# Kernel optimization log

Hardware: AMD Instinct MI355X
Metric: run time of the kernel (lower is better)

Reference implementation:

```python
import jax, jax.numpy as jnp
import numpy as np

N = 131072      # total nodes
B = 512         # number of graphs
F_DIM = 512     # in_channels
H = F_DIM // 2  # score_net hidden
RATIO = 0.5
MARGIN = 0.5
TOPK_LOSS_WEIGHT = 0.2


def setup_inputs() -> dict:
    key = jax.random.key(0)
    k1, k2, k3 = jax.random.split(key, 3)
    x = jax.random.normal(k1, (N, F_DIM), dtype=jnp.float32)
    # sorted segment ids: equal-sized graphs of N // B nodes
    batch = (jnp.arange(N) // (N // B)).astype(jnp.int32)
    W1 = jax.random.normal(k2, (F_DIM, H), dtype=jnp.float32) / np.sqrt(F_DIM).astype(np.float32)
    b1 = jnp.zeros((H,), dtype=jnp.float32)
    W2 = jax.random.normal(k3, (H, 1), dtype=jnp.float32) / np.sqrt(H).astype(np.float32)
    b2 = jnp.zeros((1,), dtype=jnp.float32)
    return {"x": x, "batch": batch, "W1": W1, "b1": b1, "W2": W2, "b2": b2}


def reference(x, batch, W1, b1, W2, b2):
    # scores = score_net(x).squeeze(-1)   [N]
    scores = (jax.nn.relu(x @ W1 + b1) @ W2 + b2)[:, 0]

    # per-graph node counts and k = max(1, int(ratio * n_i))
    counts = jax.ops.segment_sum(jnp.ones((N,), dtype=scores.dtype), batch, num_segments=B)
    k = jnp.maximum(1, jnp.floor(RATIO * counts).astype(jnp.int32))  # [B]

    # segmented top-k via lexsort: sort by (batch asc, score desc)
    order = jnp.lexsort((-scores, batch))          # [N] permutation
    b_sorted = batch[order]
    starts = jnp.cumsum(counts) - counts           # exclusive-cumsum segment starts
    rank = jnp.arange(N, dtype=counts.dtype) - starts[b_sorted]  # rank within graph (0 = highest score)
    sel_sorted = rank < k[b_sorted].astype(counts.dtype)
    selected_mask = jnp.zeros((N,), dtype=bool).at[order].set(sel_sorted)

    # global_add_pool over selected nodes
    m = selected_mask.astype(x.dtype)
    x_pooled = jax.ops.segment_sum(x * m[:, None], batch, num_segments=B)  # [B, F]

    # margin regularization loss per graph
    sel_cnt = jax.ops.segment_sum(m, batch, num_segments=B)
    sel_sum = jax.ops.segment_sum(scores * m, batch, num_segments=B)
    tot_sum = jax.ops.segment_sum(scores, batch, num_segments=B)
    uns_cnt = counts - sel_cnt
    sel_mean = sel_sum / jnp.maximum(sel_cnt, 1.0)
    uns_mean = (tot_sum - sel_sum) / jnp.maximum(uns_cnt, 1.0)
    per_graph = jnp.where(uns_cnt > 0, jax.nn.relu(MARGIN - (sel_mean - uns_mean)), 0.0)
    topk_loss = per_graph.sum() / B * TOPK_LOSS_WEIGHT

    return x_pooled, topk_loss, selected_mask
```

## Files before the change

### kernel.cpp

```cpp
#include <hip/hip_runtime.h>

#define N_NODES 131072
#define BGRAPHS 512
#define FDIM    512
#define HDIM    256
#define NPG     256
#define KSEL    128
#define STAGES  16
#define STAGE_UNITS 3072
#define STAGE_BYTES (STAGE_UNITS * 16)

typedef __attribute__((ext_vector_type(8)))  short bf16x8;
typedef __attribute__((ext_vector_type(16))) float f32x16;

__device__ __forceinline__ unsigned short bf16_rne(float f, float* back) {
    unsigned u = __float_as_uint(f);
    unsigned r = u + 0x7FFFu + ((u >> 16) & 1u);
    unsigned short h = (unsigned short)(r >> 16);
    *back = __uint_as_float(((unsigned)h) << 16);
    return h;
}

__global__ __launch_bounds__(256)
void split_w1_kernel(const float* __restrict__ W1, unsigned short* __restrict__ wsB)
{
    const int uid  = blockIdx.x * 256 + threadIdx.x;
    const int lane = uid & 63;
    int t = uid >> 6;
    const int nt = t & 7;  t >>= 3;
    const int q  = t & 1;  t >>= 1;
    const int p  = t % 3;
    const int s  = t / 3;
    const int n  = nt * 32 + (lane & 31);
    const int k0 = s * 32 + q * 16 + (lane >> 5) * 8;

    bf16x8 v;
    #pragma unroll
    for (int j = 0; j < 8; ++j) {
        float w = W1[(size_t)(k0 + j) * HDIM + n];
        float f1, f2, f3;
        unsigned short h1 = bf16_rne(w, &f1);
        float r1 = w - f1;
        unsigned short h2 = bf16_rne(r1, &f2);
        float r2 = r1 - f2;
        unsigned short h3 = bf16_rne(r2, &f3);
        v[j] = (short)(p == 0 ? h1 : (p == 1 ? h2 : h3));
    }
    *(bf16x8*)(wsB + (size_t)uid * 8) = v;
}

__global__ __launch_bounds__(512, 2)
void fused_kernel(const float* __restrict__ x,
                  const unsigned short* __restrict__ wsB,
                  const float* __restrict__ b1, const float* __restrict__ W2,
                  const float* __restrict__ b2,
                  float* __restrict__ pooled, float* __restrict__ mask_out,
                  float* __restrict__ loss_per_g)
{
    __shared__ unsigned short ldsB[STAGE_BYTES / 2];
    __shared__ float Sp[2][NPG];
    __shared__ float sv[NPG];
    __shared__ int   selr[KSEL];
    __shared__ float redT[NPG];
    __shared__ float redS[NPG];

    const int g    = blockIdx.x;
    const int tid  = threadIdx.x;
    const int lane = tid & 63;
    const int wv   = tid >> 6;
    const int wy   = wv & 3;
    const int wx   = wv >> 2;
    const int l31  = lane & 31;
    const int lh   = lane >> 5;
    const int m_base = g * NPG + wy * 64;

    f32x16 acc[2][4];
    #pragma unroll
    for (int a = 0; a < 2; ++a)
        #pragma unroll
        for (int b = 0; b < 4; ++b)
            #pragma unroll
            for (int r = 0; r < 16; ++r) acc[a][b][r] = 0.f;

    for (int s = 0; s < STAGES; ++s) {
        __syncthreads();
        const unsigned short* src = wsB + (size_t)s * (STAGE_BYTES / 2);
        #pragma unroll
        for (int i = 0; i < 6; ++i) {
            const int unit = i * 512 + tid;
            __builtin_amdgcn_global_load_lds(
                (const __attribute__((address_space(1))) unsigned int*)(src + (size_t)unit * 8),
                (__attribute__((address_space(3))) unsigned int*)(ldsB + unit * 8),
                16, 0, 0);
        }
        __syncthreads();

        #pragma unroll
        for (int q = 0; q < 2; ++q) {
            float4 xa[2], xb[2];
            #pragma unroll
            for (int mt = 0; mt < 2; ++mt) {
                const int row = m_base + mt * 32 + l31;
                const float* xp = x + (size_t)row * FDIM + s * 32 + q * 16 + lh * 8;
                xa[mt] = *(const float4*)xp;
                xb[mt] = *(const float4*)(xp + 4);
            }
            const bf16x8* bfp = (const bf16x8*)ldsB;
            bf16x8 Bh[4], Bm[4], Bl[4];
            #pragma unroll
            for (int nt = 0; nt < 4; ++nt) {
                const int nn = wx * 4 + nt;
                Bh[nt] = bfp[((0 * 2 + q) * 8 + nn) * 64 + lane];
                Bm[nt] = bfp[((1 * 2 + q) * 8 + nn) * 64 + lane];
                Bl[nt] = bfp[((2 * 2 + q) * 8 + nn) * 64 + lane];
            }
            #pragma unroll
            for (int mt = 0; mt < 2; ++mt) {
                float v[8] = {xa[mt].x, xa[mt].y, xa[mt].z, xa[mt].w,
                              xb[mt].x, xb[mt].y, xb[mt].z, xb[mt].w};
                bf16x8 Ah, Am, Al;
                #pragma unroll
                for (int j = 0; j < 8; ++j) {
                    float f1, f2, f3;
                    unsigned short h1 = bf16_rne(v[j], &f1);
                    float r1 = v[j] - f1;
                    unsigned short h2 = bf16_rne(r1, &f2);
                    float r2 = r1 - f2;
                    unsigned short h3 = bf16_rne(r2, &f3);
                    Ah[j] = (short)h1; Am[j] = (short)h2; Al[j] = (short)h3;
                }
                #pragma unroll
                for (int nt = 0; nt < 4; ++nt) {
                    acc[mt][nt] = __builtin_amdgcn_mfma_f32_32x32x16_bf16(Ah, Bh[nt], acc[mt][nt], 0, 0, 0);
                    acc[mt][nt] = __builtin_amdgcn_mfma_f32_32x32x16_bf16(Ah, Bm[nt], acc[mt][nt], 0, 0, 0);
                    acc[mt][nt] = __builtin_amdgcn_mfma_f32_32x32x16_bf16(Am, Bh[nt], acc[mt][nt], 0, 0, 0);
                    acc[mt][nt] = __builtin_amdgcn_mfma_f32_32x32x16_bf16(Ah, Bl[nt], acc[mt][nt], 0, 0, 0);
                    acc[mt][nt] = __builtin_amdgcn_mfma_f32_32x32x16_bf16(Al, Bh[nt], acc[mt][nt], 0, 0, 0);
                    acc[mt][nt] = __builtin_amdgcn_mfma_f32_32x32x16_bf16(Am, Bm[nt], acc[mt][nt], 0, 0, 0);
                }
            }
        }
    }

    float bb[4], ww[4];
    #pragma unroll
    for (int nt = 0; nt < 4; ++nt) {
        const int c = wx * 128 + nt * 32 + l31;
        bb[nt] = b1[c];
        ww[nt] = W2[c];
    }
    #pragma unroll
    for (int mt = 0; mt < 2; ++mt) {
        float pr[16];
        #pragma unroll
        for (int r = 0; r < 16; ++r) pr[r] = 0.f;
        #pragma unroll
        for (int nt = 0; nt < 4; ++nt)
            #pragma unroll
            for (int r = 0; r < 16; ++r) {
                float h = acc[mt][nt][r] + bb[nt];
                h = h > 0.f ? h : 0.f;
                pr[r] = fmaf(h, ww[nt], pr[r]);
            }
        #pragma unroll
        for (int mask = 1; mask <= 16; mask <<= 1)
            #pragma unroll
            for (int r = 0; r < 16; ++r)
                pr[r] += __shfl_xor(pr[r], mask);
        if (l31 == 0) {
            #pragma unroll
            for (int r = 0; r < 16; ++r) {
                const int row = wy * 64 + mt * 32 + (r & 3) + 8 * (r >> 2) + 4 * lh;
                Sp[wx][row] = pr[r];
            }
        }
    }
    __syncthreads();

    float sc = 0.f;
    if (tid < NPG) {
        sc = b2[0] + Sp[0][tid] + Sp[1][tid];
        sv[tid] = sc;
    }
    __syncthreads();

    bool sel = false;
    if (tid < NPG) {
        int rank = 0;
        for (int j = 0; j < NPG; ++j) {
            const float sj = sv[j];
            rank += (sj > sc || (sj == sc && j < tid)) ? 1 : 0;
        }
        sel = rank < KSEL;
        mask_out[g * NPG + tid] = sel ? 1.0f : 0.0f;
        if (sel) selr[rank] = tid;
        redT[tid] = sc;
        redS[tid] = sel ? sc : 0.f;
    }
    __syncthreads();

    for (int off = 128; off > 0; off >>= 1) {
        if (tid < off) { redT[tid] += redT[tid + off]; redS[tid] += redS[tid + off]; }
        __syncthreads();
    }
    if (tid == 0) {
        const float tot = redT[0], ssum = redS[0];
        const float sel_mean = ssum * (1.0f / KSEL);
        const float uns_mean = (tot - ssum) * (1.0f / (NPG - KSEL));
        const float v = 0.5f - (sel_mean - uns_mean);
        loss_per_g[g] = v > 0.f ? v : 0.f;
    }

    const int col = tid;
    const float* __restrict__ xg = x + (size_t)g * NPG * FDIM;
    float a0 = 0.f, a1 = 0.f, a2 = 0.f, a3 = 0.f;
    #pragma unroll 4
    for (int n = 0; n < KSEL; n += 4) {
        a0 += xg[(size_t)selr[n + 0] * FDIM + col];
        a1 += xg[(size_t)selr[n + 1] * FDIM + col];
        a2 += xg[(size_t)selr[n + 2] * FDIM + col];
        a3 += xg[(size_t)selr[n + 3] * FDIM + col];
    }
    pooled[g * FDIM + col] = (a0 + a1) + (a2 + a3);
}

__global__ __launch_bounds__(256)
void loss_kernel(const float* __restrict__ loss_per_g, float* __restrict__ out_loss)
{
    __shared__ float red[256];
    const int t = threadIdx.x;
    red[t] = loss_per_g[t] + loss_per_g[t + 256];
    __syncthreads();
    for (int off = 128; off > 0; off >>= 1) {
        if (t < off) red[t] += red[t + off];
        __syncthreads();
    }
    if (t == 0) out_loss[0] = red[0] * (0.2f / BGRAPHS);
}

extern "C" void kernel_launch(void* const* d_in, const int* in_sizes, int n_in,
                              void* d_out, int out_size, void* d_ws, size_t ws_size,
                              hipStream_t stream)
{
    const float* x  = (const float*)d_in[0];
    const float* W1 = (const float*)d_in[2];
    const float* b1 = (const float*)d_in[3];
    const float* W2 = (const float*)d_in[4];
    const float* b2 = (const float*)d_in[5];

    float* out    = (float*)d_out;
    float* pooled = out;
    float* loss   = out + BGRAPHS * FDIM;
    float* mask   = loss + 1;

    float* loss_g       = (float*)d_ws;
    unsigned short* wsB = (unsigned short*)((char*)d_ws + 4096);

    split_w1_kernel<<<192, 256, 0, stream>>>(W1, wsB);
    fused_kernel<<<BGRAPHS, 512, 0, stream>>>(x, wsB, b1, W2, b2,
                                              pooled, mask, loss_g);
    loss_kernel<<<1, 256, 0, stream>>>(loss_g, loss);
}
```

Before: 506.4 us.

## Double-buffer W1 stages and split x into bf16 planes once in LDS

The W1 bf16 stage buffer is now double-buffered, so loads for the next K-stage are issued before the current stage's MFMAs. Each x element is now split into three bf16 planes once per block and stored in padded LDS tiles. Previously the two column-half waves each split the same x elements, so this removes duplicated conversion work and duplicated global loads. The cost is much more LDS per block (about 157 KB), which likely allows only one block per CU instead of two. The W1 prepack layout is also reordered so each stage's planes sit next to each other.

```diff
diff --git a/kernel.cpp b/kernel.cpp
--- a/kernel.cpp
+++ b/kernel.cpp
@@ -7,8 +7,9 @@
 #define NPG     256
 #define KSEL    128
 #define STAGES  16
-#define STAGE_UNITS 3072
-#define STAGE_BYTES (STAGE_UNITS * 16)
+#define BSTAGE_SHORTS 24576
+#define A_ROW   40
+#define A_PLANE (NPG * A_ROW)
 
 typedef __attribute__((ext_vector_type(8)))  short bf16x8;
 typedef __attribute__((ext_vector_type(16))) float f32x16;
@@ -28,9 +29,9 @@
     const int lane = uid & 63;
     int t = uid >> 6;
     const int nt = t & 7;  t >>= 3;
-    const int q  = t & 1;  t >>= 1;
-    const int p  = t % 3;
-    const int s  = t / 3;
+    const int p  = t % 3;  t /= 3;
+    const int q  = t & 1;
+    const int s  = t >> 1;
     const int n  = nt * 32 + (lane & 31);
     const int k0 = s * 32 + q * 16 + (lane >> 5) * 8;
 
@@ -57,12 +58,8 @@
                   float* __restrict__ pooled, float* __restrict__ mask_out,
                   float* __restrict__ loss_per_g)
 {
-    __shared__ unsigned short ldsB[STAGE_BYTES / 2];
-    __shared__ float Sp[2][NPG];
-    __shared__ float sv[NPG];
-    __shared__ int   selr[KSEL];
-    __shared__ float redT[NPG];
-    __shared__ float redS[NPG];
+    __shared__ __attribute__((aligned(16))) unsigned char smem[2 * 49152 + 3 * A_PLANE * 2];
+    unsigned short* ldsA = (unsigned short*)(smem + 2 * 49152);
 
     const int g    = blockIdx.x;
     const int tid  = threadIdx.x;
@@ -72,7 +69,10 @@
     const int wx   = wv >> 2;
     const int l31  = lane & 31;
     const int lh   = lane >> 5;
-    const int m_base = g * NPG + wy * 64;
+
+    const int r  = tid >> 1;
+    const int hf = tid & 1;
+    const float* aptr = x + ((size_t)(g * NPG + r)) * FDIM + hf * 16;
 
     f32x16 acc[2][4];
     #pragma unroll
@@ -80,55 +80,96 @@
         #pragma unroll
         for (int b = 0; b < 4; ++b)
             #pragma unroll
-            for (int r = 0; r < 16; ++r) acc[a][b][r] = 0.f;
-
-    for (int s = 0; s < STAGES; ++s) {
-        __syncthreads();
-        const unsigned short* src = wsB + (size_t)s * (STAGE_BYTES / 2);
+            for (int rr = 0; rr < 16; ++rr) acc[a][b][rr] = 0.f;
+
+    float4 pf0, pf1, pf2, pf3;
+
+    pf0 = *(const float4*)(aptr + 0);
+    pf1 = *(const float4*)(aptr + 4);
+    pf2 = *(const float4*)(aptr + 8);
+    pf3 = *(const float4*)(aptr + 12);
+    {
+        const unsigned short* src = wsB;
         #pragma unroll
         for (int i = 0; i < 6; ++i) {
             const int unit = i * 512 + tid;
             __builtin_amdgcn_global_load_lds(
                 (const __attribute__((address_space(1))) unsigned int*)(src + (size_t)unit * 8),
-                (__attribute__((address_space(3))) unsigned int*)(ldsB + unit * 8),
+                (__attribute__((address_space(3))) unsigned int*)((unsigned short*)smem + unit * 8),
                 16, 0, 0);
         }
-        __syncthreads();
-
+    }
+    {
+        float v[16] = {pf0.x, pf0.y, pf0.z, pf0.w, pf1.x, pf1.y, pf1.z, pf1.w,
+                       pf2.x, pf2.y, pf2.z, pf2.w, pf3.x, pf3.y, pf3.z, pf3.w};
+        unsigned short H[16], M[16], L[16];
+        #pragma unroll
+        for (int j = 0; j < 16; ++j) {
+            float f1, f2, f3;
+            H[j] = bf16_rne(v[j], &f1);
+            float r1 = v[j] - f1;
+            M[j] = bf16_rne(r1, &f2);
+            float r2 = r1 - f2;
+            L[j] = bf16_rne(r2, &f3);
+        }
+        const int base = r * A_ROW + hf * 16;
+        const unsigned short* P[3] = {H, M, L};
+        #pragma unroll
+        for (int p = 0; p < 3; ++p) {
+            const unsigned short* s8 = P[p];
+            uint4 u0, u1;
+            u0.x = (unsigned)s8[0] | ((unsigned)s8[1] << 16);
+            u0.y = (unsigned)s8[2] | ((unsigned)s8[3] << 16);
+            u0.z = (unsigned)s8[4] | ((unsigned)s8[5] << 16);
+            u0.w = (unsigned)s8[6] | ((unsigned)s8[7] << 16);
+            u1.x = (unsigned)s8[8] | ((unsigned)s8[9] << 16);
+            u1.y = (unsigned)s8[10] | ((unsigned)s8[11] << 16);
+            u1.z = (unsigned)s8[12] | ((unsigned)s8[13] << 16);
+            u1.w = (unsigned)s8[14] | ((unsigned)s8[15] << 16);
+            uint4* dst = (uint4*)(ldsA + p * A_PLANE + base);
+            dst[0] = u0;
+            dst[1] = u1;
+        }
+    }
+    __syncthreads();
+
+    for (int s = 0; s < STAGES; ++s) {
+        if (s < STAGES - 1) {
+            const unsigned short* src = wsB + (size_t)(s + 1) * BSTAGE_SHORTS;
+            unsigned short* dstB = (unsigned short*)smem + ((s + 1) & 1) * BSTAGE_SHORTS;
+            #pragma unroll
+            for (int i = 0; i < 6; ++i) {
+                const int unit = i * 512 + tid;
+                __builtin_amdgcn_global_load_lds(
+                    (const __attribute__((address_space(1))) unsigned int*)(src + (size_t)unit * 8),
+                    (__attribute__((address_space(3))) unsigned int*)(dstB + unit * 8),
+                    16, 0, 0);
+            }
+            const float* ap = aptr + (s + 1) * 32;
+            pf0 = *(const float4*)(ap + 0);
+            pf1 = *(const float4*)(ap + 4);
+            pf2 = *(const float4*)(ap + 8);
+            pf3 = *(const float4*)(ap + 12);
+        }
+
+        const bf16x8* bfp = (const bf16x8*)((unsigned short*)smem + (s & 1) * BSTAGE_SHORTS);
         #pragma unroll
         for (int q = 0; q < 2; ++q) {
-            float4 xa[2], xb[2];
-            #pragma unroll
-            for (int mt = 0; mt < 2; ++mt) {
-                const int row = m_base + mt * 32 + l31;
-                const float* xp = x + (size_t)row * FDIM + s * 32 + q * 16 + lh * 8;
-                xa[mt] = *(const float4*)xp;
-                xb[mt] = *(const float4*)(xp + 4);
-            }
-            const bf16x8* bfp = (const bf16x8*)ldsB;
             bf16x8 Bh[4], Bm[4], Bl[4];
             #pragma unroll
             for (int nt = 0; nt < 4; ++nt) {
                 const int nn = wx * 4 + nt;
-                Bh[nt] = bfp[((0 * 2 + q) * 8 + nn) * 64 + lane];
-                Bm[nt] = bfp[((1 * 2 + q) * 8 + nn) * 64 + lane];
-                Bl[nt] = bfp[((2 * 2 + q) * 8 + nn) * 64 + lane];
+                Bh[nt] = bfp[((q * 3 + 0) * 8 + nn) * 64 + lane];
+                Bm[nt] = bfp[((q * 3 + 1) * 8 + nn) * 64 + lane];
+                Bl[nt] = bfp[((q * 3 + 2) * 8 + nn) * 64 + lane];
             }
             #pragma unroll
             for (int mt = 0; mt < 2; ++mt) {
-                float v[8] = {xa[mt].x, xa[mt].y, xa[mt].z, xa[mt].w,
-                              xb[mt].x, xb[mt].y, xb[mt].z, xb[mt].w};
-                bf16x8 Ah, Am, Al;
-                #pragma unroll
-                for (int j = 0; j < 8; ++j) {
-                    float f1, f2, f3;
-                    unsigned short h1 = bf16_rne(v[j], &f1);
-                    float r1 = v[j] - f1;
-                    unsigned short h2 = bf16_rne(r1, &f2);
-                    float r2 = r1 - f2;
-                    unsigned short h3 = bf16_rne(r2, &f3);
-                    Ah[j] = (short)h1; Am[j] = (short)h2; Al[j] = (short)h3;
-                }
+                const int m = wy * 64 + mt * 32 + l31;
+                const int aoff = m * A_ROW + q * 16 + lh * 8;
+                bf16x8 Ah = *(const bf16x8*)(ldsA + 0 * A_PLANE + aoff);
+                bf16x8 Am = *(const bf16x8*)(ldsA + 1 * A_PLANE + aoff);
+                bf16x8 Al = *(const bf16x8*)(ldsA + 2 * A_PLANE + aoff);
                 #pragma unroll
                 for (int nt = 0; nt < 4; ++nt) {
                     acc[mt][nt] = __builtin_amdgcn_mfma_f32_32x32x16_bf16(Ah, Bh[nt], acc[mt][nt], 0, 0, 0);
@@ -140,7 +181,48 @@
                 }
             }
         }
-    }
+        __syncthreads();
+
+        if (s < STAGES - 1) {
+            float v[16] = {pf0.x, pf0.y, pf0.z, pf0.w, pf1.x, pf1.y, pf1.z, pf1.w,
+                           pf2.x, pf2.y, pf2.z, pf2.w, pf3.x, pf3.y, pf3.z, pf3.w};
+            unsigned short H[16], M[16], L[16];
+            #pragma unroll
+            for (int j = 0; j < 16; ++j) {
+                float f1, f2, f3;
+                H[j] = bf16_rne(v[j], &f1);
+                float r1 = v[j] - f1;
+                M[j] = bf16_rne(r1, &f2);
+                float r2 = r1 - f2;
+                L[j] = bf16_rne(r2, &f3);
+            }
+            const int base = r * A_ROW + hf * 16;
+            const unsigned short* P[3] = {H, M, L};
+            #pragma unroll
+            for (int p = 0; p < 3; ++p) {
+                const unsigned short* s8 = P[p];
+                uint4 u0, u1;
+                u0.x = (unsigned)s8[0] | ((unsigned)s8[1] << 16);
+                u0.y = (unsigned)s8[2] | ((unsigned)s8[3] << 16);
+                u0.z = (unsigned)s8[4] | ((unsigned)s8[5] << 16);
+                u0.w = (unsigned)s8[6] | ((unsigned)s8[7] << 16);
+                u1.x = (unsigned)s8[8] | ((unsigned)s8[9] << 16);
+                u1.y = (unsigned)s8[10] | ((unsigned)s8[11] << 16);
+                u1.z = (unsigned)s8[12] | ((unsigned)s8[13] << 16);
+                u1.w = (unsigned)s8[14] | ((unsigned)s8[15] << 16);
+                uint4* dst = (uint4*)(ldsA + p * A_PLANE + base);
+                dst[0] = u0;
+                dst[1] = u1;
+            }
+        }
+        __syncthreads();
+    }
+
+    float* Sp   = (float*)smem;
+    float* sv   = Sp + 2 * NPG;
+    int*   selr = (int*)(sv + NPG);
+    float* redT = (float*)(selr + KSEL);
+    float* redS = redT + NPG;
 
     float bb[4], ww[4];
     #pragma unroll
@@ -153,25 +235,25 @@
     for (int mt = 0; mt < 2; ++mt) {
         float pr[16];
         #pragma unroll
-        for (int r = 0; r < 16; ++r) pr[r] = 0.f;
+        for (int rr = 0; rr < 16; ++rr) pr[rr] = 0.f;
         #pragma unroll
         for (int nt = 0; nt < 4; ++nt)
             #pragma unroll
-            for (int r = 0; r < 16; ++r) {
-                float h = acc[mt][nt][r] + bb[nt];
+            for (int rr = 0; rr < 16; ++rr) {
+                float h = acc[mt][nt][rr] + bb[nt];
                 h = h > 0.f ? h : 0.f;
-                pr[r] = fmaf(h, ww[nt], pr[r]);
+                pr[rr] = fmaf(h, ww[nt], pr[rr]);
             }
         #pragma unroll
         for (int mask = 1; mask <= 16; mask <<= 1)
             #pragma unroll
-            for (int r = 0; r < 16; ++r)
-                pr[r] += __shfl_xor(pr[r], mask);
+            for (int rr = 0; rr < 16; ++rr)
+                pr[rr] += __shfl_xor(pr[rr], mask);
         if (l31 == 0) {
             #pragma unroll
-            for (int r = 0; r < 16; ++r) {
-                const int row = wy * 64 + mt * 32 + (r & 3) + 8 * (r >> 2) + 4 * lh;
-                Sp[wx][row] = pr[r];
+            for (int rr = 0; rr < 16; ++rr) {
+                const int row = wy * 64 + mt * 32 + (rr & 3) + 8 * (rr >> 2) + 4 * lh;
+                Sp[wx * NPG + row] = pr[rr];
             }
         }
     }
@@ -179,19 +261,18 @@
 
     float sc = 0.f;
     if (tid < NPG) {
-        sc = b2[0] + Sp[0][tid] + Sp[1][tid];
+        sc = b2[0] + Sp[tid] + Sp[NPG + tid];
         sv[tid] = sc;
     }
     __syncthreads();
 
-    bool sel = false;
     if (tid < NPG) {
         int rank = 0;
         for (int j = 0; j < NPG; ++j) {
             const float sj = sv[j];
             rank += (sj > sc || (sj == sc && j < tid)) ? 1 : 0;
         }
-        sel = rank < KSEL;
+        const bool sel = rank < KSEL;
         mask_out[g * NPG + tid] = sel ? 1.0f : 0.0f;
         if (sel) selr[rank] = tid;
         redT[tid] = sc;
```

New measurement: 476.5 us. 5.9% less time.

## Drop LDS staging of W1 splits and read B fragments directly from global

Applied to the files above, without the earlier changes.

Removes the per-stage global_load_lds copy of the split W1 fragments and its two __syncthreads, so each wave loads its B fragments straight from global memory (L2-resident, 768KB total). The split kernel's layout is reordered so the three precision parts for a given q sit next to each other, making per-wave reads contiguous. This cuts barrier stalls and LDS traffic, which should also allow more occupancy. The cost is redundant global/L2 reads of B across the four wy waves and across blocks, plus possibly higher load latency.

```diff
diff --git a/kernel.cpp b/kernel.cpp
--- a/kernel.cpp
+++ b/kernel.cpp
@@ -7,8 +7,7 @@
 #define NPG     256
 #define KSEL    128
 #define STAGES  16
-#define STAGE_UNITS 3072
-#define STAGE_BYTES (STAGE_UNITS * 16)
+#define BSTAGE_UNITS 3072
 
 typedef __attribute__((ext_vector_type(8)))  short bf16x8;
 typedef __attribute__((ext_vector_type(16))) float f32x16;
@@ -21,6 +20,21 @@
     return h;
 }
 
+__device__ __forceinline__ void split8(const float4& a, const float4& b,
+                                       bf16x8& H, bf16x8& M, bf16x8& L) {
+    float v[8] = {a.x, a.y, a.z, a.w, b.x, b.y, b.z, b.w};
+    #pragma unroll
+    for (int j = 0; j < 8; ++j) {
+        float f1, f2, f3;
+        unsigned short h1 = bf16_rne(v[j], &f1);
+        float r1 = v[j] - f1;
+        unsigned short h2 = bf16_rne(r1, &f2);
+        float r2 = r1 - f2;
+        unsigned short h3 = bf16_rne(r2, &f3);
+        H[j] = (short)h1; M[j] = (short)h2; L[j] = (short)h3;
+    }
+}
+
 __global__ __launch_bounds__(256)
 void split_w1_kernel(const float* __restrict__ W1, unsigned short* __restrict__ wsB)
 {
@@ -28,9 +42,9 @@
     const int lane = uid & 63;
     int t = uid >> 6;
     const int nt = t & 7;  t >>= 3;
-    const int q  = t & 1;  t >>= 1;
-    const int p  = t % 3;
-    const int s  = t / 3;
+    const int p  = t % 3;  t /= 3;
+    const int q  = t & 1;
+    const int s  = t >> 1;
     const int n  = nt * 32 + (lane & 31);
     const int k0 = s * 32 + q * 16 + (lane >> 5) * 8;
 
@@ -57,8 +71,7 @@
                   float* __restrict__ pooled, float* __restrict__ mask_out,
                   float* __restrict__ loss_per_g)
 {
-    __shared__ unsigned short ldsB[STAGE_BYTES / 2];
-    __shared__ float Sp[2][NPG];
+    __shared__ float Sp[2 * NPG];
     __shared__ float sv[NPG];
     __shared__ int   selr[KSEL];
     __shared__ float redT[NPG];
@@ -72,7 +85,9 @@
     const int wx   = wv >> 2;
     const int l31  = lane & 31;
     const int lh   = lane >> 5;
-    const int m_base = g * NPG + wy * 64;
+
+    const float* aRow0 = x + (size_t)(g * NPG + wy * 64 + l31) * FDIM;
+    const float* aRow1 = aRow0 + (size_t)32 * FDIM;
 
     f32x16 acc[2][4];
     #pragma unroll
@@ -80,64 +95,45 @@
         #pragma unroll
         for (int b = 0; b < 4; ++b)
             #pragma unroll
-            for (int r = 0; r < 16; ++r) acc[a][b][r] = 0.f;
+            for (int rr = 0; rr < 16; ++rr) acc[a][b][rr] = 0.f;
 
     for (int s = 0; s < STAGES; ++s) {
-        __syncthreads();
-        const unsigned short* src = wsB + (size_t)s * (STAGE_BYTES / 2);
-        #pragma unroll
-        for (int i = 0; i < 6; ++i) {
-            const int unit = i * 512 + tid;
-            __builtin_amdgcn_global_load_lds(
-                (const __attribute__((address_space(1))) unsigned int*)(src + (size_t)unit * 8),
-                (__attribute__((address_space(3))) unsigned int*)(ldsB + unit * 8),
-                16, 0, 0);
-        }
-        __syncthreads();
-
         #pragma unroll
         for (int q = 0; q < 2; ++q) {
-            float4 xa[2], xb[2];
-            #pragma unroll
-            for (int mt = 0; mt < 2; ++mt) {
-                const int row = m_base + mt * 32 + l31;
-                const float* xp = x + (size_t)row * FDIM + s * 32 + q * 16 + lh * 8;
-                xa[mt] = *(const float4*)xp;
-                xb[mt] = *(const float4*)(xp + 4);
-            }
-            const bf16x8* bfp = (const bf16x8*)ldsB;
+            const int ko = s * 32 + q * 16 + lh * 8;
+            const float4 xa0 = *(const float4*)(aRow0 + ko);
+            const float4 xb0 = *(const float4*)(aRow0 + ko + 4);
+            const float4 xa1 = *(const float4*)(aRow1 + ko);
+            const float4 xb1 = *(const float4*)(aRow1 + ko + 4);
+            const bf16x8* Bq = (const bf16x8*)wsB
+                             + (size_t)s * BSTAGE_UNITS + q * 3 * 512 + wx * 4 * 64 + lane;
             bf16x8 Bh[4], Bm[4], Bl[4];
             #pragma unroll
             for (int nt = 0; nt < 4; ++nt) {
-                const int nn = wx * 4 + nt;
-                Bh[nt] = bfp[((0 * 2 + q) * 8 + nn) * 64 + lane];
-                Bm[nt] = bfp[((1 * 2 + q) * 8 + nn) * 64 + lane];
-                Bl[nt] = bfp[((2 * 2 + q) * 8 + nn) * 64 + lane];
-            }
-            #pragma unroll
-            for (int mt = 0; mt < 2; ++mt) {
-                float v[8] = {xa[mt].x, xa[mt].y, xa[mt].z, xa[mt].w,
-                              xb[mt].x, xb[mt].y, xb[mt].z, xb[mt].w};
-                bf16x8 Ah, Am, Al;
-                #pragma unroll
-                for (int j = 0; j < 8; ++j) {
-                    float f1, f2, f3;
-                    unsigned short h1 = bf16_rne(v[j], &f1);
-                    float r1 = v[j] - f1;
-                    unsigned short h2 = bf16_rne(r1, &f2);
-                    float r2 = r1 - f2;
-                    unsigned short h3 = bf16_rne(r2, &f3);
-                    Ah[j] = (short)h1; Am[j] = (short)h2; Al[j] = (short)h3;
-                }
-                #pragma unroll
-                for (int nt = 0; nt < 4; ++nt) {
-                    acc[mt][nt] = __builtin_amdgcn_mfma_f32_32x32x16_bf16(Ah, Bh[nt], acc[mt][nt], 0, 0, 0);
-                    acc[mt][nt] = __builtin_amdgcn_mfma_f32_32x32x16_bf16(Ah, Bm[nt], acc[mt][nt], 0, 0, 0);
-                    acc[mt][nt] = __builtin_amdgcn_mfma_f32_32x32x16_bf16(Am, Bh[nt], acc[mt][nt], 0, 0, 0);
-                    acc[mt][nt] = __builtin_amdgcn_mfma_f32_32x32x16_bf16(Ah, Bl[nt], acc[mt][nt], 0, 0, 0);
-                    acc[mt][nt] = __builtin_amdgcn_mfma_f32_32x32x16_bf16(Al, Bh[nt], acc[mt][nt], 0, 0, 0);
-                    acc[mt][nt] = __builtin_amdgcn_mfma_f32_32x32x16_bf16(Am, Bm[nt], acc[mt][nt], 0, 0, 0);
-                }
+                Bh[nt] = Bq[nt * 64];
+                Bm[nt] = Bq[512 + nt * 64];
+                Bl[nt] = Bq[1024 + nt * 64];
+            }
+            bf16x8 Ah0, Am0, Al0, Ah1, Am1, Al1;
+            split8(xa0, xb0, Ah0, Am0, Al0);
+            split8(xa1, xb1, Ah1, Am1, Al1);
+            #pragma unroll
+            for (int nt = 0; nt < 4; ++nt) {
+                acc[0][nt] = __builtin_amdgcn_mfma_f32_32x32x16_bf16(Ah0, Bh[nt], acc[0][nt], 0, 0, 0);
+                acc[0][nt] = __builtin_amdgcn_mfma_f32_32x32x16_bf16(Ah0, Bm[nt], acc[0][nt], 0, 0, 0);
+                acc[0][nt] = __builtin_amdgcn_mfma_f32_32x32x16_bf16(Am0, Bh[nt], acc[0][nt], 0, 0, 0);
+                acc[0][nt] = __builtin_amdgcn_mfma_f32_32x32x16_bf16(Ah0, Bl[nt], acc[0][nt], 0, 0, 0);
+                acc[0][nt] = __builtin_amdgcn_mfma_f32_32x32x16_bf16(Al0, Bh[nt], acc[0][nt], 0, 0, 0);
+                acc[0][nt] = __builtin_amdgcn_mfma_f32_32x32x16_bf16(Am0, Bm[nt], acc[0][nt], 0, 0, 0);
+            }
+            #pragma unroll
+            for (int nt = 0; nt < 4; ++nt) {
+                acc[1][nt] = __builtin_amdgcn_mfma_f32_32x32x16_bf16(Ah1, Bh[nt], acc[1][nt], 0, 0, 0);
+                acc[1][nt] = __builtin_amdgcn_mfma_f32_32x32x16_bf16(Ah1, Bm[nt], acc[1][nt], 0, 0, 0);
+                acc[1][nt] = __builtin_amdgcn_mfma_f32_32x32x16_bf16(Am1, Bh[nt], acc[1][nt], 0, 0, 0);
+                acc[1][nt] = __builtin_amdgcn_mfma_f32_32x32x16_bf16(Ah1, Bl[nt], acc[1][nt], 0, 0, 0);
+                acc[1][nt] = __builtin_amdgcn_mfma_f32_32x32x16_bf16(Al1, Bh[nt], acc[1][nt], 0, 0, 0);
+                acc[1][nt] = __builtin_amdgcn_mfma_f32_32x32x16_bf16(Am1, Bm[nt], acc[1][nt], 0, 0, 0);
             }
         }
     }
@@ -153,25 +149,25 @@
     for (int mt = 0; mt < 2; ++mt) {
         float pr[16];
         #pragma unroll
-        for (int r = 0; r < 16; ++r) pr[r] = 0.f;
+        for (int rr = 0; rr < 16; ++rr) pr[rr] = 0.f;
         #pragma unroll
         for (int nt = 0; nt < 4; ++nt)
             #pragma unroll
-            for (int r = 0; r < 16; ++r) {
-                float h = acc[mt][nt][r] + bb[nt];
+            for (int rr = 0; rr < 16; ++rr) {
+                float h = acc[mt][nt][rr] + bb[nt];
                 h = h > 0.f ? h : 0.f;
-                pr[r] = fmaf(h, ww[nt], pr[r]);
+                pr[rr] = fmaf(h, ww[nt], pr[rr]);
             }
         #pragma unroll
         for (int mask = 1; mask <= 16; mask <<= 1)
             #pragma unroll
-            for (int r = 0; r < 16; ++r)
-                pr[r] += __shfl_xor(pr[r], mask);
+            for (int rr = 0; rr < 16; ++rr)
+                pr[rr] += __shfl_xor(pr[rr], mask);
         if (l31 == 0) {
             #pragma unroll
-            for (int r = 0; r < 16; ++r) {
-                const int row = wy * 64 + mt * 32 + (r & 3) + 8 * (r >> 2) + 4 * lh;
-                Sp[wx][row] = pr[r];
+            for (int rr = 0; rr < 16; ++rr) {
+                const int row = wy * 64 + mt * 32 + (rr & 3) + 8 * (rr >> 2) + 4 * lh;
+                Sp[wx * NPG + row] = pr[rr];
             }
         }
     }
@@ -179,19 +175,18 @@
 
     float sc = 0.f;
     if (tid < NPG) {
-        sc = b2[0] + Sp[0][tid] + Sp[1][tid];
+        sc = b2[0] + Sp[tid] + Sp[NPG + tid];
         sv[tid] = sc;
     }
     __syncthreads();
 
-    bool sel = false;
     if (tid < NPG) {
         int rank = 0;
         for (int j = 0; j < NPG; ++j) {
             const float sj = sv[j];
             rank += (sj > sc || (sj == sc && j < tid)) ? 1 : 0;
         }
-        sel = rank < KSEL;
+        const bool sel = rank < KSEL;
         mask_out[g * NPG + tid] = sel ? 1.0f : 0.0f;
         if (sel) selr[rank] = tid;
         redT[tid] = sc;
```

Result: no change. 508.8 us (+0.5%).
